# Kernel optimization log

Hardware: AMD Instinct MI355X
Metric: run time of the kernel (lower is better)

The kernel has to match this reference:

```python
import jax, jax.numpy as jnp
import numpy as np


def _conv(x, w, b=None, stride=1, pad=0):
    # x: [N,C,H,W], w: [O,I,kh,kw]
    out = jax.lax.conv_general_dilated(
        x, w, (stride, stride), [(pad, pad), (pad, pad)],
        dimension_numbers=('NCHW', 'OIHW', 'NCHW'))
    return out if b is None else out + b[None, :, None, None]


def _cond_net(x, cw1, cb1, cw2, cb2, cw3, cb3):
    # ZeroPad2d(1) + conv(pad=0) == conv(pad=1)
    h = jax.nn.relu(_conv(x, cw1, cb1, stride=2, pad=1))
    h = jax.nn.relu(_conv(h, cw2, cb2, stride=2, pad=1))
    h = jax.nn.relu(_conv(h, cw3, cb3, stride=2, pad=1))
    return h.mean(axis=(2, 3))  # [B, 32]


def _hda(x, dyn_w, ow, share_w, share_b):
    # per-sample dynamic conv: weight[b] = dyn_w * ow[b]
    B = x.shape[0]
    w = dyn_w[None] * ow.reshape(B, *dyn_w.shape)  # [B,32,64,3,3]
    out1 = jax.vmap(lambda xb, wb: _conv(xb[None], wb, pad=1)[0])(x, w)
    out2 = _conv(x, share_w, share_b, pad=1)
    return jnp.concatenate([out1, out2], axis=1)  # [B,64,H,W]


def setup_inputs() -> dict:
    key = jax.random.key(0)
    ks = jax.random.split(key, 20)
    s = 0.05
    inp = {
        'x': jax.random.normal(ks[0], (8, 64, 256, 256), jnp.float32),
        'out_weight1': jax.random.normal(ks[1], (256, 64, 3, 3), jnp.float32),
        'out_weight2': jax.random.normal(ks[2], (256, 64, 3, 3), jnp.float32),
        # Condition_tp params
        'cw1': jax.random.normal(ks[3], (32, 64, 7, 7), jnp.float32) * s,
        'cb1': jnp.zeros((32,), jnp.float32),
        'cw2': jax.random.normal(ks[4], (32, 32, 3, 3), jnp.float32) * s,
        'cb2': jnp.zeros((32,), jnp.float32),
        'cw3': jax.random.normal(ks[5], (32, 32, 3, 3), jnp.float32) * s,
        'cb3': jnp.zeros((32,), jnp.float32),
        # FiLM linears (cond_nf=32 -> base_nf=64)
        'scale_w': jax.random.normal(ks[6], (64, 32), jnp.float32) * s,
        'scale_b': jnp.zeros((64,), jnp.float32),
        'shift_w': jax.random.normal(ks[7], (64, 32), jnp.float32) * s,
        'shift_b': jnp.zeros((64,), jnp.float32),
        # HDA_conv 1
        'dyn1_w': jax.random.normal(ks[8], (32, 64, 3, 3), jnp.float32) * s,
        'share1_w': jax.random.normal(ks[9], (32, 64, 3, 3), jnp.float32) * s,
        'share1_b': jnp.zeros((32,), jnp.float32),
        # HDA_conv 2
        'dyn2_w': jax.random.normal(ks[10], (32, 64, 3, 3), jnp.float32) * s,
        'share2_w': jax.random.normal(ks[11], (32, 64, 3, 3), jnp.float32) * s,
        'share2_b': jnp.zeros((32,), jnp.float32),
    }
    return inp


def reference(x, out_weight1, out_weight2, cw1, cb1, cw2, cb2, cw3, cb3,
              scale_w, scale_b, shift_w, shift_b,
              dyn1_w, share1_w, share1_b, dyn2_w, share2_w, share2_b):
    res_scale = 1.0
    cond = _cond_net(x, cw1, cb1, cw2, cb2, cw3, cb3)       # [B,32]
    scale = cond @ scale_w.T + scale_b                      # [B,64]
    shift = cond @ shift_w.T + shift_b                      # [B,64]
    out = _hda(x, dyn1_w, out_weight1, share1_w, share1_b)  # [B,64,H,W]
    # out*scale + shift + out  ==  out*(scale+1) + shift
    out = out * (scale[:, :, None, None] + 1.0) + shift[:, :, None, None]
    out = jax.nn.relu(out)
    out = _hda(out, dyn2_w, out_weight2, share2_w, share2_b)
    return x + out * res_scale
```

## Files before the change

### kernel.cpp

```cpp
#include <hip/hip_runtime.h>

typedef unsigned short u16;
typedef unsigned int u32;
typedef __attribute__((ext_vector_type(8))) __bf16 bf16x8;
typedef __attribute__((ext_vector_type(8))) u16 u16x8;
typedef __attribute__((ext_vector_type(4))) float f32x4;
typedef __attribute__((ext_vector_type(2))) u32 u32x2;

static constexpr size_t PS = (size_t)8 * 256 * 256 * 16;

__device__ __forceinline__ u16 f2bf(float f) {
  u32 u = __builtin_bit_cast(u32, f);
  u = (u + 0x7FFFu + ((u >> 16) & 1u)) >> 16;
  return (u16)u;
}

__device__ __forceinline__ f32x4 mfma16(bf16x8 a, bf16x8 b, f32x4 c) {
  return __builtin_amdgcn_mfma_f32_16x16x32_bf16(a, b, c, 0, 0, 0);
}

__global__ __launch_bounds__(256) void k_tr(const float* __restrict__ x,
                                            u16* __restrict__ xh) {
  __shared__ float t[64][33];
  const int b = blockIdx.z, y = blockIdx.y, x0 = blockIdx.x * 32;
  const int tid = threadIdx.x;
  {
    int ic = tid >> 2, xo = (tid & 3) * 8;
    const float* s = x + (((size_t)b * 64 + ic) * 256 + y) * 256 + x0 + xo;
    f32x4 v0 = *(const f32x4*)s;
    f32x4 v1 = *(const f32x4*)(s + 4);
#pragma unroll
    for (int j = 0; j < 4; ++j) { t[ic][xo + j] = v0[j]; t[ic][xo + 4 + j] = v1[j]; }
  }
  __syncthreads();
  {
    int xc = tid & 31, slot = tid >> 5;
    int ic0 = slot * 8;
    u16x8 v;
#pragma unroll
    for (int j = 0; j < 8; ++j) v[j] = f2bf(t[ic0 + j][xc]);
    *(u16x8*)(xh + (size_t)(slot >> 1) * PS +
              (((size_t)b * 256 + y) * 256 + x0 + xc) * 16 + (slot & 1) * 8) = v;
  }
}

__global__ void k_prep_cw(const float* __restrict__ src, u16* __restrict__ dst,
                          int IC, int KK2, int n, int perm) {
  int d = blockIdx.x * 256 + threadIdx.x;
  if (d >= n) return;
  int per = KK2 * IC;
  int oc = d / per, r = d - oc * per;
  int tap = r / IC, icp = r - tap * IC;
  int ic = perm ? ((icp >> 1) + (icp & 1) * 16) : icp;
  dst[d] = f2bf(src[(oc * IC + ic) * KK2 + tap]);
}

__global__ void k_prep_cw1(const float* __restrict__ src, u16* __restrict__ dst) {
  int d = blockIdx.x * 256 + threadIdx.x;
  if (d >= 106496) return;
  int h = d / 13312, r = d - h * 13312;
  int oc = r / 416, r2 = r - oc * 416;
  int tap = r2 >> 3, i = r2 & 7;
  float v = (tap < 49) ? src[(oc * 64 + h * 8 + i) * 49 + tap] : 0.f;
  dst[d] = f2bf(v);
}

__global__ void k_prep_hda(const float* __restrict__ dyn, const float* __restrict__ ow,
                           const float* __restrict__ share, const float* __restrict__ a_,
                           u16* __restrict__ dst, int use_a, int perm) {
  int d = blockIdx.x * 256 + threadIdx.x;
  if (d >= 8 * 64 * 576) return;
  int b = d / 36864, r = d - b * 36864;
  int oc = r / 576, k = r - oc * 576;
  int tap = k >> 6, icp = k & 63;
  int ic = perm ? ((icp & 3) * 16 + (icp >> 2)) : icp;
  float v = (oc < 32) ? dyn[(oc * 64 + ic) * 9 + tap] * ow[((b * 32 + oc) * 64 + ic) * 9 + tap]
                      : share[((oc - 32) * 64 + ic) * 9 + tap];
  if (use_a) v *= a_[b * 64 + oc];
  dst[d] = f2bf(v);
}

__global__ __launch_bounds__(256, 3) void k_cond1_mfma(const u16* __restrict__ xh,
    const u16* __restrict__ wp , const float* __restrict__ cb,
    u16* __restrict__ dst) {
  __shared__ char lds[49664];
  const int wg0 = blockIdx.x;
  const int wg = ((wg0 & 7) << 6) | (wg0 >> 3);
  const int b = wg >> 6, rr = wg & 63;
  const int oh0 = (rr >> 3) << 4, ow0 = (rr & 7) << 4;
  const int tid = threadIdx.x, lane = tid & 63, wid = tid >> 6;
  const int col = lane & 15, kq = lane >> 4;
  const int ihs = 2 * oh0 - 1, iws = 2 * ow0 - 1;
  const u16x8 Z = (u16x8)0;
  f32x4 acc[4][2];
#pragma unroll
  for (int i = 0; i < 4; ++i)
#pragma unroll
    for (int j = 0; j < 2; ++j) acc[i][j] = 0.f;
  int pb[4];
#pragma unroll
  for (int mf = 0; mf < 4; ++mf) pb[mf] = (2 * (wid * 4 + mf)) * 37 + 2 * col;
  const int wl = 22528 + col * 848 + kq * 16;
#pragma unroll 1
  for (int h = 0; h < 8; ++h) {
    __syncthreads();
    for (int i = tid; i < 1406; i += 256) {
      int r = i / 37, cc = i - r * 37;
      int gy = ihs + r, gx = iws + cc;
      u16x8 v = Z;
      if ((unsigned)gy < 256u && (unsigned)gx < 256u)
        v = *(const u16x8*)(xh + (size_t)(h >> 1) * PS +
                            (((size_t)b * 256 + gy) * 256 + gx) * 16 + (h & 1) * 8);
      *(u16x8*)(lds + (i ^ ((i >> 3) & 7)) * 16) = v;
    }
    for (int i = tid; i < 1664; i += 256) {
      int oc = i / 52, t = i - oc * 52;
      u16x8 v = *(const u16x8*)(wp + h * 13312 + oc * 416 + t * 8);
      *(u16x8*)(lds + 22528 + oc * 848 + t * 16) = v;
    }
    __syncthreads();
#pragma unroll
    for (int s = 0; s < 13; ++s) {
      const int t0 = 4 * s;
      const int kh0 = t0 / 7, r7 = t0 % 7;
      int carry = (kq >= 7 - r7) ? 1 : 0;
      int kh = kh0 + carry;
      int kw = r7 + kq - carry * 7;
      int prow = kh * 37 + kw;
      bf16x8 a[4];
#pragma unroll
      for (int mf = 0; mf < 4; ++mf) {
        int pos = pb[mf] + prow;
        int g = pos ^ ((pos >> 3) & 7);
        a[mf] = __builtin_bit_cast(bf16x8, *(const u16x8*)(lds + g * 16));
      }
      bf16x8 w[2];
#pragma unroll
      for (int nf = 0; nf < 2; ++nf)
        w[nf] = __builtin_bit_cast(bf16x8, *(const u16x8*)(lds + wl + nf * 13568 + s * 64));
#pragma unroll
      for (int mf = 0; mf < 4; ++mf)
#pragma unroll
        for (int nf = 0; nf < 2; ++nf) acc[mf][nf] = mfma16(a[mf], w[nf], acc[mf][nf]);
    }
  }
  const float bv0 = cb[col], bv1 = cb[16 + col];
#pragma unroll
  for (int mf = 0; mf < 4; ++mf) {
    int oh = oh0 + wid * 4 + mf;
    if (oh >= 126) continue;
#pragma unroll
    for (int r = 0; r < 4; ++r) {
      int ow = ow0 + kq * 4 + r;
      if (ow >= 126) continue;
      u32 pack = (u32)f2bf(fmaxf(acc[mf][0][r] + bv0, 0.f)) |
                 ((u32)f2bf(fmaxf(acc[mf][1][r] + bv1, 0.f)) << 16);
      *(u32*)(dst + (((size_t)b * 126 + oh) * 126 + ow) * 32 + col * 2) = pack;
    }
  }
}

template <int HI, int HO, int IC, int KK, int OUTF32>
__global__ __launch_bounds__(256, 4) void k_conv_s2(const u16* __restrict__ src,
    const u16* __restrict__ wgt, const float* __restrict__ bias, void* __restrict__ dst) {
  const int b = blockIdx.z;
  const int by0 = blockIdx.y * 8, bx0 = blockIdx.x * 16;
  const int tid = threadIdx.x, lane = tid & 63, wid = tid >> 6;
  const int col = lane & 15, kq = lane >> 4;
  f32x4 acc[2][2];
#pragma unroll
  for (int i = 0; i < 2; ++i)
#pragma unroll
    for (int j = 0; j < 2; ++j) acc[i][j] = 0.f;
  const u16x8 Z = (u16x8)0;
#pragma unroll
  for (int kh = 0; kh < KK; ++kh) {
#pragma unroll
    for (int kw = 0; kw < KK; ++kw) {
#pragma unroll
      for (int h = 0; h < IC / 32; ++h) {
        bf16x8 a[2];
#pragma unroll
        for (int mf = 0; mf < 2; ++mf) {
          int oh = by0 + wid * 2 + mf;
          int ih = 2 * oh - 1 + kh;
          int ix = 2 * (bx0 + col) - 1 + kw;
          int ic = h * 32 + kq * 8;
          u16x8 raw = Z;
          if ((unsigned)ih < (unsigned)HI && (unsigned)ix < (unsigned)HI)
            raw = *(const u16x8*)(src + (((size_t)b * HI + ih) * HI + ix) * IC + ic);
          a[mf] = __builtin_bit_cast(bf16x8, raw);
        }
        int k0 = (kh * KK + kw) * IC + h * 32 + kq * 8;
        bf16x8 w[2];
#pragma unroll
        for (int nf = 0; nf < 2; ++nf)
          w[nf] = __builtin_bit_cast(bf16x8,
                    *(const u16x8*)(wgt + (size_t)(nf * 16 + col) * (KK * KK * IC) + k0));
#pragma unroll
        for (int mf = 0; mf < 2; ++mf)
#pragma unroll
          for (int nf = 0; nf < 2; ++nf) acc[mf][nf] = mfma16(a[mf], w[nf], acc[mf][nf]);
      }
    }
  }
#pragma unroll
  for (int mf = 0; mf < 2; ++mf) {
    int oh = by0 + wid * 2 + mf;
    if (oh >= HO) continue;
#pragma unroll
    for (int nf = 0; nf < 2; ++nf) {
      int oc = nf * 16 + col;
      float bv = bias[oc];
#pragma unroll
      for (int r = 0; r < 4; ++r) {
        int ow = bx0 + kq * 4 + r;
        if (ow >= HO) continue;
        float v = fmaxf(acc[mf][nf][r] + bv, 0.f);
        if (OUTF32)
          ((float*)dst)[(((size_t)b * 32 + oc) * HO + oh) * HO + ow] = v;
        else
          ((u16*)dst)[(((size_t)b * HO + oh) * HO + ow) * 32 + oc] = f2bf(v);
      }
    }
  }
}

__global__ void k_mean(const float* __restrict__ h3, float* __restrict__ cond) {
  int bo = blockIdx.x;
  int tid = threadIdx.x;
  float s = 0.f;
  for (int i = tid; i < 1024; i += 256) s += h3[bo * 1024 + i];
  __shared__ float red[256];
  red[tid] = s;
  __syncthreads();
  for (int o = 128; o > 0; o >>= 1) {
    if (tid < o) red[tid] += red[tid + o];
    __syncthreads();
  }
  if (tid == 0) cond[bo] = red[0] * (1.f / 1024.f);
}

__global__ void k_film(const float* __restrict__ cond,
                       const float* __restrict__ scale_w, const float* __restrict__ scale_b,
                       const float* __restrict__ shift_w, const float* __restrict__ shift_b,
                       const float* __restrict__ share1_b, const float* __restrict__ share2_b,
                       float* __restrict__ a_, float* __restrict__ bias1,
                       float* __restrict__ bias2) {
  int t = threadIdx.x;
  int b = t >> 6, j = t & 63;
  float s = scale_b[j], sh = shift_b[j];
  for (int k = 0; k < 32; ++k) {
    float c = cond[b * 32 + k];
    s = fmaf(c, scale_w[j * 32 + k], s);
    sh = fmaf(c, shift_w[j * 32 + k], sh);
  }
  float a = s + 1.f;
  float b0 = (j < 32) ? 0.f : share1_b[j - 32];
  a_[t] = a;
  bias1[t] = fmaf(a, b0, sh);
  bias2[t] = (j < 32) ? 0.f : share2_b[j - 32];
}

template <int STAGE>
__global__ __launch_bounds__(256, 2) void k_hda_mfma(const u16* __restrict__ asrc,
    const u16* __restrict__ wall, const float* __restrict__ bias,
    const float* __restrict__ resid, void* __restrict__ dst) {
  __shared__ char lds[79360];
  const int wg0 = blockIdx.x;
  const int wg = ((wg0 & 7) << 8) + (wg0 >> 3);
  const int b = wg >> 8;
  const int rr = wg & 255;
  const int by0 = (rr >> 4) << 4, bx0 = (rr & 15) << 4;
  const int tid = threadIdx.x, lane = tid & 63, wid = tid >> 6;
  const int col = lane & 15, kq = lane >> 4;
  const u16x8 Z = (u16x8)0;
  const u16* wb = wall + (size_t)b * 64 * 576;
  for (int i = tid; i < 2592; i += 256) {
    int L = i >> 3, c = i & 7;
    int yy = L / 18, xx = L - yy * 18;
    int gy = by0 - 1 + yy, gx = bx0 - 1 + xx;
    u16x8 v = Z;
    if ((unsigned)gy < 256u && (unsigned)gx < 256u)
      v = *(const u16x8*)(asrc + (size_t)(c >> 1) * PS +
                          (((size_t)b * 256 + gy) * 256 + gx) * 16 + (c & 1) * 8);
    int off = (L * 128 + c * 16) ^ ((L & 7) << 4);
    *(u16x8*)(lds + off) = v;
  }
  {
    int i = tid;
#pragma unroll
    for (int it = 0; it < 9; ++it, i += 256) {
      int oc = i / 36, s = i - oc * 36;
      int tap = s >> 2, q = s & 3;
      u16x8 v = *(const u16x8*)(wb + oc * 576 + tap * 64 + q * 8);
      int off = 41472 + oc * 592 + s * 16;
      *(u16x8*)(lds + off) = v;
    }
  }
  __syncthreads();
  f32x4 acc[4][4];
#pragma unroll
  for (int i = 0; i < 4; ++i)
#pragma unroll
    for (int j = 0; j < 4; ++j) acc[i][j] = 0.f;
#pragma unroll 1
  for (int h = 0; h < 2; ++h) {
    if (h == 1) {
      __syncthreads();
      int i = tid;
#pragma unroll
      for (int it = 0; it < 9; ++it, i += 256) {
        int oc = i / 36, s = i - oc * 36;
        int tap = s >> 2, q = s & 3;
        u16x8 v = *(const u16x8*)(wb + oc * 576 + tap * 64 + 32 + q * 8);
        int off = 41472 + oc * 592 + s * 16;
        *(u16x8*)(lds + off) = v;
      }
      __syncthreads();
    }
#pragma unroll
    for (int tap = 0; tap < 9; ++tap) {
      const int kh = tap / 3, kw = tap - kh * 3;
      bf16x8 a[4];
#pragma unroll
      for (int mf = 0; mf < 4; ++mf) {
        int L = (wid * 4 + mf + kh) * 18 + (col + kw);
        int off = (L * 128 + h * 64 + kq * 16) ^ ((L & 7) << 4);
        a[mf] = __builtin_bit_cast(bf16x8, *(const u16x8*)(lds + off));
      }
      bf16x8 w[4];
#pragma unroll
      for (int nf = 0; nf < 4; ++nf) {
        int oc = nf * 16 + col;
        int off = 41472 + oc * 592 + (tap * 4 + kq) * 16;
        w[nf] = __builtin_bit_cast(bf16x8, *(const u16x8*)(lds + off));
      }
#pragma unroll
      for (int mf = 0; mf < 4; ++mf)
#pragma unroll
        for (int nf = 0; nf < 4; ++nf) acc[mf][nf] = mfma16(a[mf], w[nf], acc[mf][nf]);
    }
  }
  const float* bb = bias + b * 64;
#pragma unroll
  for (int mf = 0; mf < 4; ++mf) {
    int y = by0 + wid * 4 + mf;
    if (STAGE == 1) {
#pragma unroll
      for (int r = 0; r < 4; ++r) {
        int x = bx0 + kq * 4 + r;
        u32x2 pk;
        pk[0] = (u32)f2bf(fmaxf(acc[mf][0][r] + bb[col], 0.f)) |
                ((u32)f2bf(fmaxf(acc[mf][1][r] + bb[16 + col], 0.f)) << 16);
        pk[1] = (u32)f2bf(fmaxf(acc[mf][2][r] + bb[32 + col], 0.f)) |
                ((u32)f2bf(fmaxf(acc[mf][3][r] + bb[48 + col], 0.f)) << 16);
        *(u32x2*)((u16*)dst + (size_t)(col >> 2) * PS +
                  (((size_t)b * 256 + y) * 256 + x) * 16 + (col & 3) * 4) = pk;
      }
    } else {
#pragma unroll
      for (int nf = 0; nf < 4; ++nf) {
        int oc = nf * 16 + col;
        float bv = bb[oc];
        size_t o = (((size_t)b * 64 + oc) * 256 + y) * 256 + bx0 + kq * 4;
        f32x4 rx = *(const f32x4*)(resid + o);
        f32x4 vv;
#pragma unroll
        for (int r = 0; r < 4; ++r) vv[r] = rx[r] + acc[mf][nf][r] + bv;
        *(f32x4*)((float*)dst + o) = vv;
      }
    }
  }
}

extern "C" void kernel_launch(void* const* d_in, const int* in_sizes, int n_in,
                              void* d_out, int out_size, void* d_ws, size_t ws_size,
                              hipStream_t stream) {
  const float* x        = (const float*)d_in[0];
  const float* ow1      = (const float*)d_in[1];
  const float* ow2      = (const float*)d_in[2];
  const float* cw1      = (const float*)d_in[3];
  const float* cb1      = (const float*)d_in[4];
  const float* cw2      = (const float*)d_in[5];
  const float* cb2      = (const float*)d_in[6];
  const float* cw3      = (const float*)d_in[7];
  const float* cb3      = (const float*)d_in[8];
  const float* scale_w  = (const float*)d_in[9];
  const float* scale_b  = (const float*)d_in[10];
  const float* shift_w  = (const float*)d_in[11];
  const float* shift_b  = (const float*)d_in[12];
  const float* dyn1     = (const float*)d_in[13];
  const float* share1   = (const float*)d_in[14];
  const float* share1_b = (const float*)d_in[15];
  const float* dyn2     = (const float*)d_in[16];
  const float* share2   = (const float*)d_in[17];
  const float* share2_b = (const float*)d_in[18];
  float* out = (float*)d_out;

  char* p = (char*)d_ws;
  u16* xh   = (u16*)p;            p += (size_t)8 * 256 * 256 * 64 * 2;
  u16* midh = (u16*)p;            p += (size_t)8 * 256 * 256 * 64 * 2;
  u16* wbf1 = (u16*)p;            p += (size_t)8 * 64 * 576 * 2;
  u16* wbf2 = (u16*)p;            p += (size_t)8 * 64 * 576 * 2;
  u16* cwb1 = (u16*)p;            p += (size_t)106496 * 2;
  u16* cwb2 = (u16*)p;            p += (size_t)32 * 288 * 2;
  u16* cwb3 = (u16*)p;            p += (size_t)32 * 288 * 2;
  float* a_    = (float*)p;       p += 512 * 4;
  float* bias1 = (float*)p;       p += 512 * 4;
  float* bias2 = (float*)p;       p += 512 * 4;
  float* cond  = (float*)p;       p += 256 * 4;
  u16* h1h = midh;
  u16* h2h = h1h + (size_t)8 * 126 * 126 * 32;
  float* h3 = (float*)(h2h + (size_t)8 * 63 * 63 * 32);

  k_tr<<<dim3(8, 256, 8), 256, 0, stream>>>(x, xh);

  k_prep_cw1<<<(106496 + 255) / 256, 256, 0, stream>>>(cw1, cwb1);
  k_prep_cw<<<(32 * 288 + 255) / 256, 256, 0, stream>>>(cw2, cwb2, 32, 9, 32 * 288, 1);
  k_prep_cw<<<(32 * 288 + 255) / 256, 256, 0, stream>>>(cw3, cwb3, 32, 9, 32 * 288, 0);

  k_cond1_mfma<<<512, 256, 0, stream>>>(xh, cwb1, cb1, h1h);
  k_conv_s2<126, 63, 32, 3, 0><<<dim3(4, 8, 8), 256, 0, stream>>>(h1h, cwb2, cb2, h2h);
  k_conv_s2<63, 32, 32, 3, 1><<<dim3(2, 4, 8), 256, 0, stream>>>(h2h, cwb3, cb3, h3);

  k_mean<<<256, 256, 0, stream>>>(h3, cond);
  k_film<<<1, 512, 0, stream>>>(cond, scale_w, scale_b, shift_w, shift_b,
                                share1_b, share2_b, a_, bias1, bias2);

  k_prep_hda<<<(8 * 64 * 576 + 255) / 256, 256, 0, stream>>>(dyn1, ow1, share1, a_, wbf1, 1, 0);
  k_prep_hda<<<(8 * 64 * 576 + 255) / 256, 256, 0, stream>>>(dyn2, ow2, share2, a_, wbf2, 0, 1);

  k_hda_mfma<1><<<2048, 256, 0, stream>>>(xh, wbf1, bias1, nullptr, midh);
  k_hda_mfma<2><<<2048, 256, 0, stream>>>(midh, wbf2, bias2, x, out);
}
```

Baseline: 279.8 us.

## Split HDA conv K loop into 16-channel chunks to cut LDS and raise occupancy

The HDA MFMA kernel now walks the input channels in four chunks of 16. Each chunk stages its own small input halo and weight slice into LDS, and the 9 taps are packed in pairs (padded to 10) so each MFMA covers two taps of 16 channels. The weight prep kernel writes this new chunked, padded layout. LDS per block falls from about 79KB to about 32KB and launch bounds rise to 4 blocks per CU, aiming for more latency hiding. In exchange there are more barriers and global loads per block, the padded tap wastes a tenth of the MFMA work, and register pressure is tighter.

Result: slower. 328.0 us (+17.2%).

```diff
diff --git a/kernel.cpp b/kernel.cpp
--- a/kernel.cpp
+++ b/kernel.cpp
@@ -69,14 +69,21 @@
                            const float* __restrict__ share, const float* __restrict__ a_,
                            u16* __restrict__ dst, int use_a, int perm) {
   int d = blockIdx.x * 256 + threadIdx.x;
-  if (d >= 8 * 64 * 576) return;
-  int b = d / 36864, r = d - b * 36864;
-  int oc = r / 576, k = r - oc * 576;
-  int tap = k >> 6, icp = k & 63;
-  int ic = perm ? ((icp & 3) * 16 + (icp >> 2)) : icp;
-  float v = (oc < 32) ? dyn[(oc * 64 + ic) * 9 + tap] * ow[((b * 32 + oc) * 64 + ic) * 9 + tap]
-                      : share[((oc - 32) * 64 + ic) * 9 + tap];
-  if (use_a) v *= a_[b * 64 + oc];
+  if (d >= 327680) return;
+  int b = d / 40960, r = d - b * 40960;
+  int cc = r / 10240, r2 = r - cc * 10240;
+  int oc = r2 / 160, r3 = r2 - oc * 160;
+  int s = r3 >> 5, r4 = r3 & 31;
+  int kq = r4 >> 3, j = r4 & 7;
+  int tap = 2 * s + (kq >> 1);
+  float v = 0.f;
+  if (tap < 9) {
+    int icp = cc * 16 + (kq & 1) * 8 + j;
+    int ic = perm ? ((icp & 3) * 16 + (icp >> 2)) : icp;
+    v = (oc < 32) ? dyn[(oc * 64 + ic) * 9 + tap] * ow[((b * 32 + oc) * 64 + ic) * 9 + tap]
+                  : share[((oc - 32) * 64 + ic) * 9 + tap];
+    if (use_a) v *= a_[b * 64 + oc];
+  }
   dst[d] = f2bf(v);
 }
 
@@ -263,10 +270,10 @@
 }
 
 template <int STAGE>
-__global__ __launch_bounds__(256, 2) void k_hda_mfma(const u16* __restrict__ asrc,
+__global__ __launch_bounds__(256, 4) void k_hda_mfma(const u16* __restrict__ asrc,
     const u16* __restrict__ wall, const float* __restrict__ bias,
     const float* __restrict__ resid, void* __restrict__ dst) {
-  __shared__ char lds[79360];
+  __shared__ char lds[32448];
   const int wg0 = blockIdx.x;
   const int wg = ((wg0 & 7) << 8) + (wg0 >> 3);
   const int b = wg >> 8;
@@ -274,68 +281,51 @@
   const int by0 = (rr >> 4) << 4, bx0 = (rr & 15) << 4;
   const int tid = threadIdx.x, lane = tid & 63, wid = tid >> 6;
   const int col = lane & 15, kq = lane >> 4;
+  const int hi = kq >> 1, sl = kq & 1;
   const u16x8 Z = (u16x8)0;
-  const u16* wb = wall + (size_t)b * 64 * 576;
-  for (int i = tid; i < 2592; i += 256) {
-    int L = i >> 3, c = i & 7;
-    int yy = L / 18, xx = L - yy * 18;
-    int gy = by0 - 1 + yy, gx = bx0 - 1 + xx;
-    u16x8 v = Z;
-    if ((unsigned)gy < 256u && (unsigned)gx < 256u)
-      v = *(const u16x8*)(asrc + (size_t)(c >> 1) * PS +
-                          (((size_t)b * 256 + gy) * 256 + gx) * 16 + (c & 1) * 8);
-    int off = (L * 128 + c * 16) ^ ((L & 7) << 4);
-    *(u16x8*)(lds + off) = v;
-  }
-  {
-    int i = tid;
-#pragma unroll
-    for (int it = 0; it < 9; ++it, i += 256) {
-      int oc = i / 36, s = i - oc * 36;
-      int tap = s >> 2, q = s & 3;
-      u16x8 v = *(const u16x8*)(wb + oc * 576 + tap * 64 + q * 8);
-      int off = 41472 + oc * 592 + s * 16;
-      *(u16x8*)(lds + off) = v;
-    }
-  }
-  __syncthreads();
   f32x4 acc[4][4];
 #pragma unroll
   for (int i = 0; i < 4; ++i)
 #pragma unroll
     for (int j = 0; j < 4; ++j) acc[i][j] = 0.f;
 #pragma unroll 1
-  for (int h = 0; h < 2; ++h) {
-    if (h == 1) {
-      __syncthreads();
-      int i = tid;
-#pragma unroll
-      for (int it = 0; it < 9; ++it, i += 256) {
-        int oc = i / 36, s = i - oc * 36;
-        int tap = s >> 2, q = s & 3;
-        u16x8 v = *(const u16x8*)(wb + oc * 576 + tap * 64 + 32 + q * 8);
-        int off = 41472 + oc * 592 + s * 16;
-        *(u16x8*)(lds + off) = v;
-      }
-      __syncthreads();
-    }
-#pragma unroll
-    for (int tap = 0; tap < 9; ++tap) {
-      const int kh = tap / 3, kw = tap - kh * 3;
+  for (int cc = 0; cc < 4; ++cc) {
+    const u16* ap = asrc + (size_t)cc * PS;
+    const u16* wp = wall + (size_t)b * 40960 + cc * 10240;
+    __syncthreads();
+    for (int i = tid; i < 684; i += 256) {
+      int pos = i >> 1;
+      int yy = pos / 18, xx = pos - yy * 18;
+      int gy = by0 - 1 + yy, gx = bx0 - 1 + xx;
+      u16x8 v = Z;
+      if ((unsigned)gy < 256u && (unsigned)gx < 256u)
+        v = *(const u16x8*)(ap + (((size_t)b * 256 + gy) * 256 + gx) * 16 + (i & 1) * 8);
+      *(u16x8*)(lds + (i ^ ((i >> 3) & 1)) * 16) = v;
+    }
+    for (int i = tid; i < 1280; i += 256) {
+      int oc = i / 20, t = i - oc * 20;
+      u16x8 v = *(const u16x8*)(wp + oc * 160 + t * 8);
+      *(u16x8*)(lds + 10944 + oc * 336 + t * 16) = v;
+    }
+    __syncthreads();
+#pragma unroll
+    for (int s = 0; s < 5; ++s) {
+      const int t0 = 2 * s, t1 = 2 * s + 1;
+      const int d0 = (t0 / 3) * 18 + (t0 % 3);
+      const int d1 = (t1 / 3) * 18 + (t1 % 3);
+      const int dd = hi ? d1 : d0;
       bf16x8 a[4];
 #pragma unroll
       for (int mf = 0; mf < 4; ++mf) {
-        int L = (wid * 4 + mf + kh) * 18 + (col + kw);
-        int off = (L * 128 + h * 64 + kq * 16) ^ ((L & 7) << 4);
-        a[mf] = __builtin_bit_cast(bf16x8, *(const u16x8*)(lds + off));
+        int pos = (wid * 4 + mf) * 18 + col + dd;
+        int g = (pos * 2 + sl) ^ ((pos >> 2) & 1);
+        a[mf] = __builtin_bit_cast(bf16x8, *(const u16x8*)(lds + g * 16));
       }
       bf16x8 w[4];
 #pragma unroll
-      for (int nf = 0; nf < 4; ++nf) {
-        int oc = nf * 16 + col;
-        int off = 41472 + oc * 592 + (tap * 4 + kq) * 16;
-        w[nf] = __builtin_bit_cast(bf16x8, *(const u16x8*)(lds + off));
-      }
+      for (int nf = 0; nf < 4; ++nf)
+        w[nf] = __builtin_bit_cast(bf16x8,
+            *(const u16x8*)(lds + 10944 + (nf * 16 + col) * 336 + (s * 4 + kq) * 16));
 #pragma unroll
       for (int mf = 0; mf < 4; ++mf)
 #pragma unroll
@@ -401,8 +391,8 @@
   char* p = (char*)d_ws;
   u16* xh   = (u16*)p;            p += (size_t)8 * 256 * 256 * 64 * 2;
   u16* midh = (u16*)p;            p += (size_t)8 * 256 * 256 * 64 * 2;
-  u16* wbf1 = (u16*)p;            p += (size_t)8 * 64 * 576 * 2;
-  u16* wbf2 = (u16*)p;            p += (size_t)8 * 64 * 576 * 2;
+  u16* wbf1 = (u16*)p;            p += (size_t)327680 * 2;
+  u16* wbf2 = (u16*)p;            p += (size_t)327680 * 2;
   u16* cwb1 = (u16*)p;            p += (size_t)106496 * 2;
   u16* cwb2 = (u16*)p;            p += (size_t)32 * 288 * 2;
   u16* cwb3 = (u16*)p;            p += (size_t)32 * 288 * 2;
@@ -428,8 +418,8 @@
   k_film<<<1, 512, 0, stream>>>(cond, scale_w, scale_b, shift_w, shift_b,
                                 share1_b, share2_b, a_, bias1, bias2);
 
-  k_prep_hda<<<(8 * 64 * 576 + 255) / 256, 256, 0, stream>>>(dyn1, ow1, share1, a_, wbf1, 1, 0);
-  k_prep_hda<<<(8 * 64 * 576 + 255) / 256, 256, 0, stream>>>(dyn2, ow2, share2, a_, wbf2, 0, 1);
+  k_prep_hda<<<(327680 + 255) / 256, 256, 0, stream>>>(dyn1, ow1, share1, a_, wbf1, 1, 0);
+  k_prep_hda<<<(327680 + 255) / 256, 256, 0, stream>>>(dyn2, ow2, share2, a_, wbf2, 0, 1);
 
   k_hda_mfma<1><<<2048, 256, 0, stream>>>(xh, wbf1, bias1, nullptr, midh);
   k_hda_mfma<2><<<2048, 256, 0, stream>>>(midh, wbf2, bias2, x, out);
```
